# Optimization experiments

Hardware: AMD Instinct MI355X
Metric: run time of the kernel (lower is better)

## Reference

```python
import jax, jax.numpy as jnp
import numpy as np

# ---- static config (mirrors init_kwargs) ----
EMBED_DIM = 128
NUM_HEADS = 4
N_SUB = 16       # token grid is N_SUB x N_SUB, seq = N_SUB**2
WINDOW = 4
SHIFT = 2
EPS = 1e-5
NEG_INF = -1e9


def _swin_mask(n_sub, ws, shift):
    """Standard Swin attention mask for shifted windows. [NW, T, T]."""
    img = np.zeros((n_sub, n_sub), np.int32)
    cnt = 0
    for hs in (slice(0, -ws), slice(-ws, -shift), slice(-shift, None)):
        for wsl in (slice(0, -ws), slice(-ws, -shift), slice(-shift, None)):
            img[hs, wsl] = cnt
            cnt += 1
    nw = n_sub // ws
    ids = img.reshape(nw, ws, nw, ws).transpose(0, 2, 1, 3).reshape(nw * nw, ws * ws)
    mask = np.where(ids[:, None, :] != ids[:, :, None], NEG_INF, 0.0).astype(np.float32)
    return jnp.asarray(mask)


MASK = _swin_mask(N_SUB, WINDOW, SHIFT)


def _inorm(v):
    # InstanceNorm2d (affine=False) over spatial dims, per (batch, seq, channel)
    m = v.mean(axis=(-2, -1), keepdims=True)
    var = v.var(axis=(-2, -1), keepdims=True)
    return (v - m) * jax.lax.rsqrt(var + EPS)


def _pw(x, w, b):
    # pointwise (1x1) linear over channel dim of [..., C, H, W]
    return jnp.einsum('...chw,cd->...dhw', x, w) + b[:, None, None]


def _window(x, nw, ws):
    # [B, n_sub, n_sub, C, H, W] -> [B, nw*nw, ws*ws, C, H, W]
    B = x.shape[0]
    C, H, W = x.shape[3:]
    x = x.reshape(B, nw, ws, nw, ws, C, H, W)
    return x.transpose(0, 1, 3, 2, 4, 5, 6, 7).reshape(B, nw * nw, ws * ws, C, H, W)


def _unwindow(x, nw, ws):
    B = x.shape[0]
    C, H, W = x.shape[3:]
    x = x.reshape(B, nw, nw, ws, ws, C, H, W)
    return x.transpose(0, 1, 3, 2, 4, 5, 6, 7).reshape(B, nw * ws, nw * ws, C, H, W)


def _swin_func_attn(v, w_q, b_q, w_k, b_k, w_v, b_v, w_o, b_o):
    B, S, C, H, W = v.shape
    nw = N_SUB // WINDOW
    g = v.reshape(B, N_SUB, N_SUB, C, H, W)
    if SHIFT > 0:
        g = jnp.roll(g, (-SHIFT, -SHIFT), axis=(1, 2))
    q = _window(_pw(g, w_q, b_q), nw, WINDOW)
    k = _window(_pw(g, w_k, b_k), nw, WINDOW)
    val = _window(_pw(g, w_v, b_v), nw, WINDOW)
    d = C // NUM_HEADS
    T = WINDOW * WINDOW
    split = lambda x: x.reshape(B, nw * nw, T, NUM_HEADS, d, H, W)
    q, k, val = split(q), split(k), split(val)
    # integral score: spatial mean of per-head dot products, scaled by sqrt(d)
    scale = 1.0 / (np.sqrt(d) * H * W)
    scores = jnp.einsum('bnthdxy,bnshdxy->bnhts', q, k) * scale
    scores = scores + MASK[None, :, None, :, :]
    attn = jax.nn.softmax(scores, axis=-1)
    o = jnp.einsum('bnhts,bnshdxy->bnthdxy', attn, val)
    o = o.reshape(B, nw * nw, T, C, H, W)
    o = _pw(o, w_o, b_o)
    o = _unwindow(o, nw, WINDOW)
    if SHIFT > 0:
        o = jnp.roll(o, (SHIFT, SHIFT), axis=(1, 2))
    return o.reshape(B, S, C, H, W)


def _mlp(x, w1, b1, w2, b2):
    return _pw(jax.nn.gelu(_pw(x, w1, b1)), w2, b2)


def setup_inputs() -> dict:
    key = jax.random.key(0)
    ks = jax.random.split(key, 8)
    B, S, C, H, W = 8, N_SUB * N_SUB, EMBED_DIM, 16, 16
    p = 0.02
    return {
        'v': jax.random.normal(ks[0], (B, S, C, H, W), jnp.float32),
        'w_q': jax.random.normal(ks[1], (C, C), jnp.float32) * p,
        'b_q': jnp.zeros((C,), jnp.float32),
        'w_k': jax.random.normal(ks[2], (C, C), jnp.float32) * p,
        'b_k': jnp.zeros((C,), jnp.float32),
        'w_v': jax.random.normal(ks[3], (C, C), jnp.float32) * p,
        'b_v': jnp.zeros((C,), jnp.float32),
        'w_o': jax.random.normal(ks[4], (C, C), jnp.float32) * p,
        'b_o': jnp.zeros((C,), jnp.float32),
        'w1': jax.random.normal(ks[5], (C, C), jnp.float32) * p,
        'b1': jnp.zeros((C,), jnp.float32),
        'w2': jax.random.normal(ks[6], (C, C), jnp.float32) * p,
        'b2': jnp.zeros((C,), jnp.float32),
    }


def reference(v, w_q, b_q, w_k, b_k, w_v, b_v, w_o, b_o, w1, b1, w2, b2):
    v = _swin_func_attn(_inorm(v), w_q, b_q, w_k, b_k, w_v, b_v, w_o, b_o) + v
    v = _mlp(_inorm(v), w1, b1, w2, b2) + v
    return v
```

## Files before the change

kernel.cpp:

```cpp
#include <hip/hip_runtime.h>
#include <cstdint>
#include <cstddef>

#define DI __device__ __forceinline__

typedef unsigned short u16;
typedef u16 u16x8 __attribute__((ext_vector_type(8)));
typedef u16 u16x4 __attribute__((ext_vector_type(4)));
typedef float f32x4 __attribute__((ext_vector_type(4)));
typedef __bf16 bf16x8 __attribute__((ext_vector_type(8)));

constexpr float EPSf  = 1e-5f;
constexpr float SCALE = 1.0f / (5.656854249492381f * 256.0f);

DI float bf2f(u16 u) { union { uint32_t i; float f; } v; v.i = ((uint32_t)u) << 16; return v.f; }
DI u16 f2bf(float f) {
    union { float f; uint32_t i; } v; v.f = f;
    uint32_t r = v.i + 0x7fffu + ((v.i >> 16) & 1u);
    return (u16)(r >> 16);
}

DI f32x4 MFMA(bf16x8 a, bf16x8 b, f32x4 c) {
    return __builtin_amdgcn_mfma_f32_16x16x32_bf16(a, b, c, 0, 0, 0);
}

DI int region3(int x) { return x < 12 ? 0 : (x < 14 ? 1 : 2); }

__global__ __launch_bounds__(256) void kw_prep(
        const float* __restrict__ w_q, const float* __restrict__ w_k,
        const float* __restrict__ w_v, const float* __restrict__ w_o,
        const float* __restrict__ w1,  const float* __restrict__ w2,
        u16* __restrict__ wt) {
    __shared__ float lds[128 * 129];
    const float* W;
    switch (blockIdx.x) {
        case 0: W = w_q; break; case 1: W = w_k; break; case 2: W = w_v; break;
        case 3: W = w_o; break; case 4: W = w1;  break; default: W = w2;  break;
    }
    u16* O = wt + blockIdx.x * 16384;
    int tid = threadIdx.x;
    for (int i = 0; i < 16; i++) {
        int flat = i * 1024 + tid * 4;
        float4 vv = *(const float4*)(W + flat);
        int c = flat >> 7, d = flat & 127;
        lds[c * 129 + d + 0] = vv.x; lds[c * 129 + d + 1] = vv.y;
        lds[c * 129 + d + 2] = vv.z; lds[c * 129 + d + 3] = vv.w;
    }
    __syncthreads();
    for (int i = 0; i < 32; i++) {
        int flat2 = i * 512 + tid * 2;
        int d = flat2 >> 7, c = flat2 & 127;
        u16 a = f2bf(lds[c * 129 + d]);
        u16 b = f2bf(lds[(c + 1) * 129 + d]);
        uint32_t pk = (uint32_t)a | ((uint32_t)b << 16);
        *(uint32_t*)(O + flat2) = pk;
    }
}

__global__ __launch_bounds__(512) void k2_qkv(
        const float* __restrict__ v, const u16* __restrict__ wt,
        const float* __restrict__ b_q, const float* __restrict__ b_k,
        const float* __restrict__ b_v,
        u16* __restrict__ Qg, u16* __restrict__ Kg, u16* __restrict__ Vg) {
    __shared__ u16 Abuf[256 * 136];
    __shared__ float red[2][4][128];
    __shared__ float stats[2][128];

    int tid = threadIdx.x;
    int wtk = blockIdx.x;
    int b = wtk >> 8, n = (wtk >> 4) & 15, t = wtk & 15;
    int wi = n >> 2, wj = n & 3, ti = t >> 2, tj = t & 3;
    int si = (wi * 4 + ti + 2) & 15, sj = (wj * 4 + tj + 2) & 15;
    const float* src = v + (size_t)(b * 256 + si * 16 + sj) * 32768;

    int xy = tid & 255, chh = tid >> 8;
    for (int g = 0; g < 16; g++) {
        int c0 = chh * 64 + g * 4;
        float x0 = src[(c0 + 0) * 256 + xy];
        float x1 = src[(c0 + 1) * 256 + xy];
        float x2 = src[(c0 + 2) * 256 + xy];
        float x3 = src[(c0 + 3) * 256 + xy];
        u16x4 u; u.x = f2bf(x0); u.y = f2bf(x1); u.z = f2bf(x2); u.w = f2bf(x3);
        *(u16x4*)&Abuf[xy * 136 + c0] = u;
    }
    __syncthreads();
    {
        int c = tid & 127, p = tid >> 7;
        float s = 0.f, q = 0.f;
        for (int k = 0; k < 64; k++) {
            float x = bf2f(Abuf[(p * 64 + k) * 136 + c]);
            s += x; q += x * x;
        }
        red[0][p][c] = s; red[1][p][c] = q;
    }
    __syncthreads();
    if (tid < 128) {
        int c = tid;
        float s = red[0][0][c] + red[0][1][c] + red[0][2][c] + red[0][3][c];
        float q = red[1][0][c] + red[1][1][c] + red[1][2][c] + red[1][3][c];
        float mean = s * (1.f / 256.f);
        float var = q * (1.f / 256.f) - mean * mean;
        stats[0][c] = mean; stats[1][c] = rsqrtf(var + EPSf);
    }
    __syncthreads();
    for (int g = 0; g < 16; g++) {
        int c0 = chh * 64 + g * 4;
        u16x4 u = *(u16x4*)&Abuf[xy * 136 + c0];
        u.x = f2bf((bf2f(u.x) - stats[0][c0 + 0]) * stats[1][c0 + 0]);
        u.y = f2bf((bf2f(u.y) - stats[0][c0 + 1]) * stats[1][c0 + 1]);
        u.z = f2bf((bf2f(u.z) - stats[0][c0 + 2]) * stats[1][c0 + 2]);
        u.w = f2bf((bf2f(u.w) - stats[0][c0 + 3]) * stats[1][c0 + 3]);
        *(u16x4*)&Abuf[xy * 136 + c0] = u;
    }
    __syncthreads();

    int wave = tid >> 6, lane = tid & 63;
    int lrow = lane & 15, quad = lane >> 4;
    bf16x8 afr[2][4];
    for (int mi = 0; mi < 2; mi++) {
        int mt = wave * 2 + mi;
        for (int kt = 0; kt < 4; kt++)
            afr[mi][kt] = *(const bf16x8*)&Abuf[(mt * 16 + lrow) * 136 + kt * 32 + quad * 8];
    }
    __syncthreads();
    u16* stgw = Abuf + wave * 2048;
    for (int w = 0; w < 3; w++) {
        const u16* WTp = wt + w * 16384;
        const float* bias = (w == 0) ? b_q : (w == 1) ? b_k : b_v;
        u16* O = ((w == 0) ? Qg : (w == 1) ? Kg : Vg) + (size_t)wtk * 32768;
        f32x4 acc[2][8];
        for (int mi = 0; mi < 2; mi++)
            for (int nt = 0; nt < 8; nt++) acc[mi][nt] = (f32x4){0.f, 0.f, 0.f, 0.f};
        for (int kt = 0; kt < 4; kt++) {
            for (int nt = 0; nt < 8; nt++) {
                bf16x8 bfr = *(const bf16x8*)&WTp[(nt * 16 + lrow) * 128 + kt * 32 + quad * 8];
                acc[0][nt] = MFMA(afr[0][kt], bfr, acc[0][nt]);
                acc[1][nt] = MFMA(afr[1][kt], bfr, acc[1][nt]);
            }
        }
        for (int mi = 0; mi < 2; mi++) {
            int mt = wave * 2 + mi;
            for (int nt = 0; nt < 8; nt++) {
                int d = nt * 16 + lrow;
                float bv = bias[d];
                for (int r = 0; r < 4; r++)
                    stgw[(quad * 4 + r) * 128 + d] = f2bf(acc[mi][nt][r] + bv);
            }
            __syncthreads();
            for (int ro = 0; ro < 4; ro++) {
                int flat = ro * 512 + lane * 8;
                *(u16x8*)&O[mt * 2048 + flat] = *(const u16x8*)&stgw[flat];
            }
            __syncthreads();
        }
    }
}

__global__ __launch_bounds__(256) void k3_scores(
        const u16* __restrict__ Qg, const u16* __restrict__ Kg,
        float* __restrict__ spart) {
    __shared__ u16 Qc[16 * 2056];
    __shared__ u16 Kc[16 * 2056];
    int tid = threadIdx.x;
    int bid = blockIdx.x;
    int b = bid >> 5, n = (bid >> 1) & 15, half = bid & 1;
    int wtb = (b * 16 + n) * 16;
    int lane = tid & 63, wave = tid >> 6;
    int lrow = lane & 15, quad = lane >> 4;
    f32x4 acc = {0.f, 0.f, 0.f, 0.f};
    for (int chl = 0; chl < 8; chl++) {
        int xyb = half * 128 + chl * 16;
        __syncthreads();
        for (int it = 0; it < 16; it++) {
            int flat = (it * 256 + tid) * 8;
            int tt = flat >> 11, off = flat & 2047;
            *(u16x8*)&Qc[tt * 2056 + off] =
                *(const u16x8*)&Qg[(size_t)(wtb + tt) * 32768 + xyb * 128 + off];
            *(u16x8*)&Kc[tt * 2056 + off] =
                *(const u16x8*)&Kg[(size_t)(wtb + tt) * 32768 + xyb * 128 + off];
        }
        __syncthreads();
        for (int kt = 0; kt < 16; kt++) {
            bf16x8 aq = *(const bf16x8*)&Qc[lrow * 2056 + kt * 128 + wave * 32 + quad * 8];
            bf16x8 bk = *(const bf16x8*)&Kc[lrow * 2056 + kt * 128 + wave * 32 + quad * 8];
            acc = MFMA(aq, bk, acc);
        }
    }
    float* sp = spart + (size_t)(((half * 8 + b) * 16 + n) * 4 + wave) * 256;
    for (int r = 0; r < 4; r++) sp[(quad * 4 + r) * 16 + lrow] = acc[r];
}

__global__ __launch_bounds__(512) void k4_attnout(
        const float* __restrict__ v, const u16* __restrict__ Vg,
        const float* __restrict__ spart, const u16* __restrict__ wt,
        const float* __restrict__ b_o, u16* __restrict__ v2) {
    __shared__ u16 Vc[32768];
    __shared__ u16 Obuf[256 * 136];
    __shared__ float attn[4][16][16];
    int tid = threadIdx.x;
    int bid = blockIdx.x;
    int b = bid >> 6, n = (bid >> 2) & 15, qtr = bid & 3;
    int wi = n >> 2, wj = n & 3;
    int wtb = (b * 16 + n) * 16;

    if (tid < 64) {
        int h = tid >> 4, t = tid & 15;
        int it = wi * 4 + (t >> 2) , jt = wj * 4 + (t & 3);
        int rt = region3(it) * 3 + region3(jt);
        const float* sp0 = spart + (size_t)(((0 + b) * 16 + n) * 4 + h) * 256 + t * 16;
        const float* sp1 = spart + (size_t)(((8 + b) * 16 + n) * 4 + h) * 256 + t * 16;
        float vals[16]; float mx = -1e30f;
        for (int s = 0; s < 16; s++) {
            int is = wi * 4 + (s >> 2), js = wj * 4 + (s & 3);
            int rs = region3(is) * 3 + region3(js);
            float sc = (sp0[s] + sp1[s]) * SCALE + (rs == rt ? 0.f : -1e9f);
            vals[s] = sc; mx = fmaxf(mx, sc);
        }
        float sum = 0.f;
        for (int s = 0; s < 16; s++) { vals[s] = __expf(vals[s] - mx); sum += vals[s]; }
        float inv = 1.f / sum;
        for (int s = 0; s < 16; s++) attn[h][t][s] = vals[s] * inv;
    }
    __syncthreads();

    int lane = tid & 63, wave = tid >> 6;
    int lrow = lane & 15, quad = lane >> 4;
    const u16* WoT = wt + 3 * 16384;

    for (int sub = 0; sub < 4; sub++) {
        int xyb = qtr * 64 + sub * 16;
        for (int it = 0; it < 8; it++) {
            int flat = (it * 512 + tid) * 8;
            int s = flat >> 11, rem = flat & 2047;
            *(u16x8*)&Vc[flat] =
                *(const u16x8*)&Vg[(size_t)(wtb + s) * 32768 + xyb * 128 + rem];
        }
        __syncthreads();
        {
            int c = tid & 127, xg = tid >> 7;
            int h = c >> 5;
            float vreg[4][16];
            for (int rep = 0; rep < 4; rep++) {
                int xyl = xg * 4 + rep;
                for (int s = 0; s < 16; s++)
                    vreg[rep][s] = bf2f(Vc[s * 2048 + xyl * 128 + c]);
            }
            for (int t = 0; t < 16; t++) {
                float oa0 = 0.f, oa1 = 0.f, oa2 = 0.f, oa3 = 0.f;
                for (int s = 0; s < 16; s++) {
                    float a = attn[h][t][s];
                    oa0 += a * vreg[0][s]; oa1 += a * vreg[1][s];
                    oa2 += a * vreg[2][s]; oa3 += a * vreg[3][s];
                }
                Obuf[(t * 16 + xg * 4 + 0) * 136 + c] = f2bf(oa0);
                Obuf[(t * 16 + xg * 4 + 1) * 136 + c] = f2bf(oa1);
                Obuf[(t * 16 + xg * 4 + 2) * 136 + c] = f2bf(oa2);
                Obuf[(t * 16 + xg * 4 + 3) * 136 + c] = f2bf(oa3);
            }
        }
        __syncthreads();
        bf16x8 afr[2][4];
        for (int mi = 0; mi < 2; mi++) {
            int mt = wave * 2 + mi;
            for (int kt = 0; kt < 4; kt++)
                afr[mi][kt] = *(const bf16x8*)&Obuf[(mt * 16 + lrow) * 136 + kt * 32 + quad * 8];
        }
        f32x4 acc[2][8];
        for (int mi = 0; mi < 2; mi++)
            for (int nt = 0; nt < 8; nt++) acc[mi][nt] = (f32x4){0.f, 0.f, 0.f, 0.f};
        for (int kt = 0; kt < 4; kt++) {
            for (int nt = 0; nt < 8; nt++) {
                bf16x8 bfr = *(const bf16x8*)&WoT[(nt * 16 + lrow) * 128 + kt * 32 + quad * 8];
                acc[0][nt] = MFMA(afr[0][kt], bfr, acc[0][nt]);
                acc[1][nt] = MFMA(afr[1][kt], bfr, acc[1][nt]);
            }
        }
        for (int mi = 0; mi < 2; mi++) {
            int mt = wave * 2 + mi;
            int sd = (((wi * 4 + (mt >> 2) + 2) & 15) << 4) | ((wj * 4 + (mt & 3) + 2) & 15);
            size_t tokbase = (size_t)(b * 256 + sd) * 32768;
            u16* stgw = Vc + wave * 2048;
            for (int nt = 0; nt < 8; nt++) {
                int c = nt * 16 + lrow;
                float bv = b_o[c];
                float4 res = *(const float4*)&v[tokbase + (size_t)c * 256 + xyb + quad * 4];
                stgw[(quad * 4 + 0) * 128 + c] = f2bf(acc[mi][nt][0] + bv + res.x);
                stgw[(quad * 4 + 1) * 128 + c] = f2bf(acc[mi][nt][1] + bv + res.y);
                stgw[(quad * 4 + 2) * 128 + c] = f2bf(acc[mi][nt][2] + bv + res.z);
                stgw[(quad * 4 + 3) * 128 + c] = f2bf(acc[mi][nt][3] + bv + res.w);
            }
            __syncthreads();
            size_t obase = tokbase + (size_t)xyb * 128;
            for (int ro = 0; ro < 4; ro++) {
                int flat = ro * 512 + lane * 8;
                *(u16x8*)&v2[obase + flat] = *(const u16x8*)&stgw[flat];
            }
            __syncthreads();
        }
    }
}

__global__ __launch_bounds__(512) void k6_mlp(
        const u16* __restrict__ v2, const u16* __restrict__ wt,
        const float* __restrict__ b1, const float* __restrict__ b2,
        float* __restrict__ out) {
    __shared__ u16 Nbuf[256 * 136];
    __shared__ u16 Hbuf[256 * 136];
    __shared__ float red[2][4][128];
    __shared__ float stats[3][128];
    int tid = threadIdx.x;
    size_t tok = blockIdx.x;
    const u16* src = v2 + tok * 32768;

    for (int it = 0; it < 8; it++) {
        int flat = (it * 512 + tid) * 8;
        int xy = flat >> 7, c = flat & 127;
        *(u16x8*)&Nbuf[xy * 136 + c] = *(const u16x8*)&src[flat];
    }
    __syncthreads();
    {
        int c = tid & 127, p = tid >> 7;
        float s = 0.f, q = 0.f;
        for (int k = 0; k < 64; k++) {
            float x = bf2f(Nbuf[(p * 64 + k) * 136 + c]);
            s += x; q += x * x;
        }
        red[0][p][c] = s; red[1][p][c] = q;
    }
    __syncthreads();
    if (tid < 128) {
        int c = tid;
        float s = red[0][0][c] + red[0][1][c] + red[0][2][c] + red[0][3][c];
        float q = red[1][0][c] + red[1][1][c] + red[1][2][c] + red[1][3][c];
        float mean = s * (1.f / 256.f);
        float var = q * (1.f / 256.f) - mean * mean;
        float rstd = rsqrtf(var + EPSf);
        stats[0][c] = mean; stats[1][c] = rstd; stats[2][c] = (var + EPSf) * rstd;
    }
    __syncthreads();
    {
        int c0 = (tid & 31) * 4, xyB = tid >> 5;
        for (int g = 0; g < 16; g++) {
            int xy = g * 16 + xyB;
            u16x4 u = *(u16x4*)&Nbuf[xy * 136 + c0];
            u.x = f2bf((bf2f(u.x) - stats[0][c0 + 0]) * stats[1][c0 + 0]);
            u.y = f2bf((bf2f(u.y) - stats[0][c0 + 1]) * stats[1][c0 + 1]);
            u.z = f2bf((bf2f(u.z) - stats[0][c0 + 2]) * stats[1][c0 + 2]);
            u.w = f2bf((bf2f(u.w) - stats[0][c0 + 3]) * stats[1][c0 + 3]);
            *(u16x4*)&Nbuf[xy * 136 + c0] = u;
        }
    }
    __syncthreads();

    int wave = tid >> 6, lane = tid & 63;
    int lrow = lane & 15, quad = lane >> 4;
    const u16* W1T = wt + 4 * 16384;
    const u16* W2T = wt + 5 * 16384;

    {
        bf16x8 afr[2][4];
        for (int mi = 0; mi < 2; mi++) {
            int mt = wave * 2 + mi;
            for (int kt = 0; kt < 4; kt++)
                afr[mi][kt] = *(const bf16x8*)&Nbuf[(mt * 16 + lrow) * 136 + kt * 32 + quad * 8];
        }
        f32x4 acc[2][8];
        for (int mi = 0; mi < 2; mi++)
            for (int nt = 0; nt < 8; nt++) acc[mi][nt] = (f32x4){0.f, 0.f, 0.f, 0.f};
        for (int kt = 0; kt < 4; kt++) {
            for (int nt = 0; nt < 8; nt++) {
                bf16x8 bfr = *(const bf16x8*)&W1T[(nt * 16 + lrow) * 128 + kt * 32 + quad * 8];
                acc[0][nt] = MFMA(afr[0][kt], bfr, acc[0][nt]);
                acc[1][nt] = MFMA(afr[1][kt], bfr, acc[1][nt]);
            }
        }
        for (int mi = 0; mi < 2; mi++) {
            int mt = wave * 2 + mi;
            for (int nt = 0; nt < 8; nt++) {
                int c = nt * 16 + lrow;
                float bv = b1[c];
                for (int r = 0; r < 4; r++) {
                    float x = acc[mi][nt][r] + bv;
                    float g = 0.5f * x * (1.f + tanhf(0.7978845608f * (x + 0.044715f * x * x * x)));
                    Hbuf[(mt * 16 + quad * 4 + r) * 136 + c] = f2bf(g);
                }
            }
        }
    }
    __syncthreads();
    {
        bf16x8 afr[2][4];
        for (int mi = 0; mi < 2; mi++) {
            int mt = wave * 2 + mi;
            for (int kt = 0; kt < 4; kt++)
                afr[mi][kt] = *(const bf16x8*)&Hbuf[(mt * 16 + lrow) * 136 + kt * 32 + quad * 8];
        }
        f32x4 acc[2][8];
        for (int mi = 0; mi < 2; mi++)
            for (int nt = 0; nt < 8; nt++) acc[mi][nt] = (f32x4){0.f, 0.f, 0.f, 0.f};
        for (int kt = 0; kt < 4; kt++) {
            for (int nt = 0; nt < 8; nt++) {
                bf16x8 bfr = *(const bf16x8*)&W2T[(nt * 16 + lrow) * 128 + kt * 32 + quad * 8];
                acc[0][nt] = MFMA(afr[0][kt], bfr, acc[0][nt]);
                acc[1][nt] = MFMA(afr[1][kt], bfr, acc[1][nt]);
            }
        }
        for (int mi = 0; mi < 2; mi++) {
            int mt = wave * 2 + mi;
            for (int nt = 0; nt < 8; nt++) {
                int c = nt * 16 + lrow;
                float mean = stats[0][c], sd = stats[2][c], bv = b2[c];
                f32x4 o4;
                for (int r = 0; r < 4; r++) {
                    int m = mt * 16 + quad * 4 + r;
                    float n2v = bf2f(Nbuf[m * 136 + c]);
                    o4[r] = acc[mi][nt][r] + bv + n2v * sd + mean;
                }
                *(f32x4*)&out[tok * 32768 + (size_t)c * 256 + mt * 16 + quad * 4] = o4;
            }
        }
    }
}

extern "C" void kernel_launch(void* const* d_in, const int* in_sizes, int n_in,
                              void* d_out, int out_size, void* d_ws, size_t ws_size,
                              hipStream_t stream) {
    const float* v   = (const float*)d_in[0];
    const float* w_q = (const float*)d_in[1];
    const float* b_q = (const float*)d_in[2];
    const float* w_k = (const float*)d_in[3];
    const float* b_k = (const float*)d_in[4];
    const float* w_v = (const float*)d_in[5];
    const float* b_v = (const float*)d_in[6];
    const float* w_o = (const float*)d_in[7];
    const float* b_o = (const float*)d_in[8];
    const float* w1  = (const float*)d_in[9];
    const float* b1  = (const float*)d_in[10];
    const float* w2  = (const float*)d_in[11];
    const float* b2  = (const float*)d_in[12];

    u16*   wt    = (u16*)d_ws;
    float* spart = (float*)((char*)d_ws + 196608);
    u16*   Qg    = (u16*)((char*)d_ws + 1245184);
    u16*   v2    = Qg;
    u16*   Vg    = (u16*)d_out;
    u16*   Kg    = (u16*)d_out + 67108864;
    float* out   = (float*)d_out;

    kw_prep  <<<6,    256, 0, stream>>>(w_q, w_k, w_v, w_o, w1, w2, wt);
    k2_qkv   <<<2048, 512, 0, stream>>>(v, wt, b_q, b_k, b_v, Qg, Kg, Vg);
    k3_scores<<<256,  256, 0, stream>>>(Qg, Kg, spart);
    k4_attnout<<<512, 512, 0, stream>>>(v, Vg, spart, wt, b_o, v2);
    k6_mlp   <<<2048, 512, 0, stream>>>(v2, wt, b1, b2, out);
}
```

Before: 1.216 ms.

## Stage weights in LDS, drop staging barriers, rewrite score kernel, cheaper GELU

The QKV and MLP kernels now copy each 128x128 bf16 weight tile into padded shared memory before the MFMA loops, instead of reading B fragments from global memory. The per-wave output staging buffers are now padded and disjoint, so the block-wide barriers around each store are removed in the QKV and attention-output kernels. The score kernel now uses 1024 threads that read Q and K directly from global memory and reduce partial results through shared memory, with no LDS staging. GELU's tanh form is replaced by the equivalent sigmoid form using exp and a fast reciprocal. These changes trade extra shared-memory copies and approximate-math rounding for fewer barriers and less redundant global traffic.

```diff
diff --git a/kernel.cpp b/kernel.cpp
--- a/kernel.cpp
+++ b/kernel.cpp
@@ -25,6 +25,11 @@
 }
 
 DI int region3(int x) { return x < 12 ? 0 : (x < 14 ? 1 : 2); }
+
+DI float gelu_f(float x) {
+    float u = 1.5957691216f * x * (1.f + 0.044715f * x * x);
+    return x * __builtin_amdgcn_rcpf(1.f + __expf(-u));
+}
 
 __global__ __launch_bounds__(256) void kw_prep(
         const float* __restrict__ w_q, const float* __restrict__ w_k,
@@ -74,6 +79,7 @@
     const float* src = v + (size_t)(b * 256 + si * 16 + sj) * 32768;
 
     int xy = tid & 255, chh = tid >> 8;
+    #pragma unroll 4
     for (int g = 0; g < 16; g++) {
         int c0 = chh * 64 + g * 4;
         float x0 = src[(c0 + 0) * 256 + xy];
@@ -123,17 +129,25 @@
             afr[mi][kt] = *(const bf16x8*)&Abuf[(mt * 16 + lrow) * 136 + kt * 32 + quad * 8];
     }
     __syncthreads();
-    u16* stgw = Abuf + wave * 2048;
+    u16* WTs  = Abuf;
+    u16* stgw = Abuf + 17408 + wave * 2176;
     for (int w = 0; w < 3; w++) {
         const u16* WTp = wt + w * 16384;
         const float* bias = (w == 0) ? b_q : (w == 1) ? b_k : b_v;
         u16* O = ((w == 0) ? Qg : (w == 1) ? Kg : Vg) + (size_t)wtk * 32768;
+        if (w) __syncthreads();
+        for (int i = 0; i < 4; i++) {
+            int flat = i * 4096 + tid * 8;
+            *(u16x8*)&WTs[(flat >> 7) * 136 + (flat & 127)] =
+                *(const u16x8*)&WTp[flat];
+        }
+        __syncthreads();
         f32x4 acc[2][8];
         for (int mi = 0; mi < 2; mi++)
             for (int nt = 0; nt < 8; nt++) acc[mi][nt] = (f32x4){0.f, 0.f, 0.f, 0.f};
         for (int kt = 0; kt < 4; kt++) {
             for (int nt = 0; nt < 8; nt++) {
-                bf16x8 bfr = *(const bf16x8*)&WTp[(nt * 16 + lrow) * 128 + kt * 32 + quad * 8];
+                bf16x8 bfr = *(const bf16x8*)&WTs[(nt * 16 + lrow) * 136 + kt * 32 + quad * 8];
                 acc[0][nt] = MFMA(afr[0][kt], bfr, acc[0][nt]);
                 acc[1][nt] = MFMA(afr[1][kt], bfr, acc[1][nt]);
             }
@@ -144,50 +158,48 @@
                 int d = nt * 16 + lrow;
                 float bv = bias[d];
                 for (int r = 0; r < 4; r++)
-                    stgw[(quad * 4 + r) * 128 + d] = f2bf(acc[mi][nt][r] + bv);
-            }
-            __syncthreads();
+                    stgw[(quad * 4 + r) * 136 + d] = f2bf(acc[mi][nt][r] + bv);
+            }
             for (int ro = 0; ro < 4; ro++) {
                 int flat = ro * 512 + lane * 8;
-                *(u16x8*)&O[mt * 2048 + flat] = *(const u16x8*)&stgw[flat];
-            }
-            __syncthreads();
-        }
-    }
-}
-
-__global__ __launch_bounds__(256) void k3_scores(
+                *(u16x8*)&O[mt * 2048 + flat] =
+                    *(const u16x8*)&stgw[(flat >> 7) * 136 + (flat & 127)];
+            }
+        }
+    }
+}
+
+__global__ __launch_bounds__(1024, 4) void k3_scores(
         const u16* __restrict__ Qg, const u16* __restrict__ Kg,
         float* __restrict__ spart) {
-    __shared__ u16 Qc[16 * 2056];
-    __shared__ u16 Kc[16 * 2056];
+    __shared__ f32x4 red3[3][4][64];
     int tid = threadIdx.x;
     int bid = blockIdx.x;
     int b = bid >> 5, n = (bid >> 1) & 15, half = bid & 1;
     int wtb = (b * 16 + n) * 16;
     int lane = tid & 63, wave = tid >> 6;
+    int head = wave & 3, sub = wave >> 2;
     int lrow = lane & 15, quad = lane >> 4;
+    int xyb = half * 128 + sub * 32;
+    const u16* Qp = Qg + (size_t)(wtb + lrow) * 32768 + (size_t)xyb * 128 + head * 32 + quad * 8;
+    const u16* Kp = Kg + (size_t)(wtb + lrow) * 32768 + (size_t)xyb * 128 + head * 32 + quad * 8;
     f32x4 acc = {0.f, 0.f, 0.f, 0.f};
-    for (int chl = 0; chl < 8; chl++) {
-        int xyb = half * 128 + chl * 16;
-        __syncthreads();
-        for (int it = 0; it < 16; it++) {
-            int flat = (it * 256 + tid) * 8;
-            int tt = flat >> 11, off = flat & 2047;
-            *(u16x8*)&Qc[tt * 2056 + off] =
-                *(const u16x8*)&Qg[(size_t)(wtb + tt) * 32768 + xyb * 128 + off];
-            *(u16x8*)&Kc[tt * 2056 + off] =
-                *(const u16x8*)&Kg[(size_t)(wtb + tt) * 32768 + xyb * 128 + off];
-        }
-        __syncthreads();
-        for (int kt = 0; kt < 16; kt++) {
-            bf16x8 aq = *(const bf16x8*)&Qc[lrow * 2056 + kt * 128 + wave * 32 + quad * 8];
-            bf16x8 bk = *(const bf16x8*)&Kc[lrow * 2056 + kt * 128 + wave * 32 + quad * 8];
-            acc = MFMA(aq, bk, acc);
-        }
-    }
-    float* sp = spart + (size_t)(((half * 8 + b) * 16 + n) * 4 + wave) * 256;
-    for (int r = 0; r < 4; r++) sp[(quad * 4 + r) * 16 + lrow] = acc[r];
+    #pragma unroll 4
+    for (int kt = 0; kt < 32; kt++) {
+        bf16x8 aq = *(const bf16x8*)(Qp + kt * 128);
+        bf16x8 bk = *(const bf16x8*)(Kp + kt * 128);
+        acc = MFMA(aq, bk, acc);
+    }
+    if (sub) red3[sub - 1][head][lane] = acc;
+    __syncthreads();
+    if (sub == 0) {
+        f32x4 a0 = red3[0][head][lane];
+        f32x4 a1 = red3[1][head][lane];
+        f32x4 a2 = red3[2][head][lane];
+        acc = acc + a0 + a1 + a2;
+        float* sp = spart + (size_t)(((half * 8 + b) * 16 + n) * 4 + head) * 256;
+        for (int r = 0; r < 4; r++) sp[(quad * 4 + r) * 16 + lrow] = acc[r];
+    }
 }
 
 __global__ __launch_bounds__(512) void k4_attnout(
@@ -229,6 +241,7 @@
 
     for (int sub = 0; sub < 4; sub++) {
         int xyb = qtr * 64 + sub * 16;
+        if (sub) __syncthreads();
         for (int it = 0; it < 8; it++) {
             int flat = (it * 512 + tid) * 8;
             int s = flat >> 11, rem = flat & 2047;
@@ -275,27 +288,26 @@
                 acc[1][nt] = MFMA(afr[1][kt], bfr, acc[1][nt]);
             }
         }
+        u16* stgw = Vc + wave * 2176;
         for (int mi = 0; mi < 2; mi++) {
             int mt = wave * 2 + mi;
             int sd = (((wi * 4 + (mt >> 2) + 2) & 15) << 4) | ((wj * 4 + (mt & 3) + 2) & 15);
             size_t tokbase = (size_t)(b * 256 + sd) * 32768;
-            u16* stgw = Vc + wave * 2048;
             for (int nt = 0; nt < 8; nt++) {
                 int c = nt * 16 + lrow;
                 float bv = b_o[c];
                 float4 res = *(const float4*)&v[tokbase + (size_t)c * 256 + xyb + quad * 4];
-                stgw[(quad * 4 + 0) * 128 + c] = f2bf(acc[mi][nt][0] + bv + res.x);
-                stgw[(quad * 4 + 1) * 128 + c] = f2bf(acc[mi][nt][1] + bv + res.y);
-                stgw[(quad * 4 + 2) * 128 + c] = f2bf(acc[mi][nt][2] + bv + res.z);
-                stgw[(quad * 4 + 3) * 128 + c] = f2bf(acc[mi][nt][3] + bv + res.w);
-            }
-            __syncthreads();
+                stgw[(quad * 4 + 0) * 136 + c] = f2bf(acc[mi][nt][0] + bv + res.x);
+                stgw[(quad * 4 + 1) * 136 + c] = f2bf(acc[mi][nt][1] + bv + res.y);
+                stgw[(quad * 4 + 2) * 136 + c] = f2bf(acc[mi][nt][2] + bv + res.z);
+                stgw[(quad * 4 + 3) * 136 + c] = f2bf(acc[mi][nt][3] + bv + res.w);
+            }
             size_t obase = tokbase + (size_t)xyb * 128;
             for (int ro = 0; ro < 4; ro++) {
                 int flat = ro * 512 + lane * 8;
-                *(u16x8*)&v2[obase + flat] = *(const u16x8*)&stgw[flat];
-            }
-            __syncthreads();
+                *(u16x8*)&v2[obase + flat] =
+                    *(const u16x8*)&stgw[(flat >> 7) * 136 + (flat & 127)];
+            }
         }
     }
 }
@@ -350,11 +362,17 @@
             *(u16x4*)&Nbuf[xy * 136 + c0] = u;
         }
     }
+    {
+        const u16* W1T = wt + 4 * 16384;
+        for (int i = 0; i < 4; i++) {
+            int flat = i * 4096 + tid * 8;
+            *(u16x8*)&Hbuf[(flat >> 7) * 136 + (flat & 127)] = *(const u16x8*)&W1T[flat];
+        }
+    }
     __syncthreads();
 
     int wave = tid >> 6, lane = tid & 63;
     int lrow = lane & 15, quad = lane >> 4;
-    const u16* W1T = wt + 4 * 16384;
     const u16* W2T = wt + 5 * 16384;
 
     {
@@ -369,11 +387,12 @@
             for (int nt = 0; nt < 8; nt++) acc[mi][nt] = (f32x4){0.f, 0.f, 0.f, 0.f};
         for (int kt = 0; kt < 4; kt++) {
             for (int nt = 0; nt < 8; nt++) {
-                bf16x8 bfr = *(const bf16x8*)&W1T[(nt * 16 + lrow) * 128 + kt * 32 + quad * 8];
+                bf16x8 bfr = *(const bf16x8*)&Hbuf[(nt * 16 + lrow) * 136 + kt * 32 + quad * 8];
                 acc[0][nt] = MFMA(afr[0][kt], bfr, acc[0][nt]);
                 acc[1][nt] = MFMA(afr[1][kt], bfr, acc[1][nt]);
             }
         }
+        __syncthreads();
         for (int mi = 0; mi < 2; mi++) {
             int mt = wave * 2 + mi;
             for (int nt = 0; nt < 8; nt++) {
@@ -381,13 +400,11 @@
                 float bv = b1[c];
                 for (int r = 0; r < 4; r++) {
                     float x = acc[mi][nt][r] + bv;
-                    float g = 0.5f * x * (1.f + tanhf(0.7978845608f * (x + 0.044715f * x * x * x)));
-                    Hbuf[(mt * 16 + quad * 4 + r) * 136 + c] = f2bf(g);
+                    Hbuf[(mt * 16 + quad * 4 + r) * 136 + c] = f2bf(gelu_f(x));
                 }
             }
         }
     }
-    __syncthreads();
     {
         bf16x8 afr[2][4];
         for (int mi = 0; mi < 2; mi++) {
@@ -447,9 +464,9 @@
     u16*   Kg    = (u16*)d_out + 67108864;
     float* out   = (float*)d_out;
 
-    kw_prep  <<<6,    256, 0, stream>>>(w_q, w_k, w_v, w_o, w1, w2, wt);
-    k2_qkv   <<<2048, 512, 0, stream>>>(v, wt, b_q, b_k, b_v, Qg, Kg, Vg);
-    k3_scores<<<256,  256, 0, stream>>>(Qg, Kg, spart);
-    k4_attnout<<<512, 512, 0, stream>>>(v, Vg, spart, wt, b_o, v2);
-    k6_mlp   <<<2048, 512, 0, stream>>>(v2, wt, b1, b2, out);
-}
+    kw_prep  <<<6,    256,  0, stream>>>(w_q, w_k, w_v, w_o, w1, w2, wt);
+    k2_qkv   <<<2048, 512,  0, stream>>>(v, wt, b_q, b_k, b_v, Qg, Kg, Vg);
+    k3_scores<<<256,  1024, 0, stream>>>(Qg, Kg, spart);
+    k4_attnout<<<512, 512,  0, stream>>>(v, Vg, spart, wt, b_o, v2);
+    k6_mlp   <<<2048, 512,  0, stream>>>(v2, wt, b1, b2, out);
+}
```

New measurement: 1.042 ms. 1.17x faster.
